# Kernel optimization log

Hardware: AMD Instinct MI355X
Metric: run time of the kernel (lower is better)

## Reference

```python
import jax, jax.numpy as jnp
import numpy as np

PATCH = 64
STRIDE = PATCH // 2
SEQ = 65536
NPATCH = (SEQ - PATCH) // STRIDE + 1  # 2047
B = 256
EPS = 1e-5


def setup_inputs() -> dict:
    key = jax.random.key(0)
    ks = jax.random.split(key, 10)
    s = lambda k, shp: jax.random.normal(k, shp, jnp.float32) * 0.05
    return dict(
        x=jax.random.normal(ks[0], (B, 1, SEQ), jnp.float32),
        conv1_w=s(ks[1], (NPATCH, NPATCH - 1)),
        conv1_b=s(ks[2], (NPATCH,)),
        w1=s(ks[3], (32, 3, 5)), b1=s(ks[4], (32,)),
        g1=jnp.ones((32,), jnp.float32), be1=jnp.zeros((32,), jnp.float32),
        w2=s(ks[5], (64, 32, 3)), b2=s(ks[6], (64,)),
        g2=jnp.ones((64,), jnp.float32), be2=jnp.zeros((64,), jnp.float32),
        w3=s(ks[7], (128, 64, 3)), b3=s(ks[8], (128,)),
        g3=jnp.ones((128,), jnp.float32), be3=jnp.zeros((128,), jnp.float32),
    )


def _conv1d(x, w, b, pad):
    # x: [B, Cin, L], w: [Cout, Cin, K]
    y = jax.lax.conv_general_dilated(x, w, (1,), [(pad, pad)],
                                     dimension_numbers=('NCH', 'OIH', 'NCH'))
    return y + b[None, :, None]


def _bn(x, g, be):
    # training-mode BatchNorm1d: biased var over (batch, length)
    m = jnp.mean(x, axis=(0, 2), keepdims=True)
    v = jnp.var(x, axis=(0, 2), keepdims=True)
    return (x - m) * jax.lax.rsqrt(v + EPS) * g[None, :, None] + be[None, :, None]


def _maxpool2(x):
    # MaxPool1d(kernel=2, stride=2), floor division of length
    L = x.shape[-1] // 2
    return x[..., : 2 * L].reshape(x.shape[0], x.shape[1], L, 2).max(-1)


def reference(x, conv1_w, conv1_b, w1, b1, g1, be1, w2, b2, g2, be2, w3, b3, g3, be3):
    starts = jnp.arange(NPATCH) * STRIDE
    idx = starts[:, None] + jnp.arange(PATCH)[None, :]         # [NW, W]
    xp = x[:, :, idx]                                          # [B,1,NW,W]
    mean = xp.mean(-1)                                         # [B,1,NW]
    std = jnp.std(xp, axis=-1, ddof=1)                         # torch.std is unbiased
    stats = jnp.concatenate([mean, std], axis=1)               # [B,2,NW]
    dx = jnp.diff(xp, axis=2)                                  # diff across window index: [B,1,NW-1,W]
    dmax = dx.max(-1)                                          # [B,1,NW-1]
    dmax = jnp.transpose(dmax, (0, 2, 1))                      # [B,NW-1,1]
    # conv1: 1x1 Conv1d over length-1 axis == matmul over channel dim
    d2 = jnp.einsum('oi,bil->bol', conv1_w, dmax) + conv1_b[None, :, None]  # [B,NW,1]
    d2 = jnp.transpose(d2, (0, 2, 1))                          # [B,1,NW]
    x3 = jnp.concatenate([stats, d2], axis=1)                  # [B,3,NW]
    h = _maxpool2(jax.nn.relu(_bn(_conv1d(x3, w1, b1, 2), g1, be1)))
    h = _maxpool2(jax.nn.relu(_bn(_conv1d(h, w2, b2, 1), g2, be2)))
    h = jax.nn.relu(_bn(_conv1d(h, w3, b3, 1), g3, be3))
    return h.mean(-1)                                          # AdaptiveAvgPool1d(1)+Flatten -> [B,128]
```

## Files before the change

kernel.cpp:

```cpp
#include <hip/hip_runtime.h>
#include <math.h>

#define NB 256
#define SEQ 65536
#define NP 2047
#define NPM 2046
#define NPP 2048
#define KPAD 2048
#define LEN1 2047
#define LEN2 1023
#define LEN3 511
#define C1 32
#define C2 64
#define C3 128
#define NPART 2048
#define NPART2 (NB*4)
#define SROW 40
#define SROW3 72

#define OFF_X3   0
#define SZ_X3    (NB*3*NPP)
#define OFF_DMAX (OFF_X3 + SZ_X3)
#define SZ_DMAX  (NB*NPM)
#define OFF_Y1   (OFF_DMAX + SZ_DMAX)
#define SZ_Y1    (NB*C1*LEN1)
#define OFF_Y2   (OFF_Y1 + SZ_Y1)
#define SZ_Y2    (NB*C2*LEN2)
#define OFF_S1   (OFF_Y2 + SZ_Y2)
#define OFF_S2   (OFF_S1 + 2*C1)
#define OFF_S3   (OFF_S2 + 2*C2)
#define OFF_W2C  (OFF_S3 + 2*C3)
#define OFF_W3B  (OFF_W2C + C1*C2*3)
#define OFF_PS   (OFF_W3B + C2*C3*3)
#define OFF_PQ   (OFF_PS + C3*NPART)
#define OFF_WB   OFF_Y2
#define OFF_H1R  OFF_Y2
#define OFF_PM   (OFF_Y1 + 4300000)
#define OFF_W2B  OFF_W2C

typedef __attribute__((ext_vector_type(8))) short short8;
typedef __attribute__((ext_vector_type(4))) short short4v;
typedef __attribute__((ext_vector_type(4))) float f32x4;

__device__ inline short f2bf(float f){
  union { float f; unsigned u; } x; x.f = f;
  unsigned r = x.u + 0x7FFF + ((x.u >> 16) & 1);
  return (short)(r >> 16);
}
__device__ inline float bf2f(short s){
  union { unsigned u; float f; } x; x.u = ((unsigned)(unsigned short)s) << 16; return x.f;
}

#define RED4L(v) v += __shfl_xor(v,1,64); v += __shfl_xor(v,2,64); \
                 v += __shfl_xor(v,4,64); v += __shfl_xor(v,8,64);

#define TILES(X) X(0,0) X(0,1) X(0,2) X(0,3) X(1,0) X(1,1) X(1,2) X(1,3) \
                 X(2,0) X(2,1) X(2,2) X(2,3) X(3,0) X(3,1) X(3,2) X(3,3)
#define DECLBIAS(P,ct) f32x4 bi##ct = *(const f32x4*)((P) + cbase + ct*16 + kq*4);
#define DECLACC(lt,ct) f32x4 acc##lt##ct = bi##ct;

__global__ __launch_bounds__(256) void k_pp(const float* __restrict__ x, const float* __restrict__ c1b,
                                            const float* __restrict__ W, const float* __restrict__ w2,
                                            const float* __restrict__ w3, float* __restrict__ ws){
  int bid = blockIdx.x;
  if (bid < 32*NB){
    float* x3    = ws + OFF_X3;
    short* dmaxB = (short*)(ws + OFF_DMAX);
    int b = bid >> 5;
    int chunk = bid & 31;
    const float* xr = x + (size_t)b*SEQ + chunk*2048;
    __shared__ float Ss[65], Qs[65], Dm[65];
    int w = threadIdx.x >> 6;
    int l = threadIdx.x & 63;
    #pragma unroll
    for (int i=0;i<2;i++){
      int seg = w*2 + i;
      int off = seg*256;
      float4 A = *(const float4*)(xr + off + l*4);
      float4 Bh = make_float4(0.f,0.f,0.f,0.f);
      if (l >= 56){
        int g = chunk*2048 + off + 256 + (l-56)*4;
        if (g + 3 < SEQ) Bh = *(const float4*)(xr + off + 256 + (l-56)*4);
      }
      int src = (l+8) & 63;
      float p0 = __shfl(A.x, src, 64), p1 = __shfl(A.y, src, 64),
            p2 = __shfl(A.z, src, 64), p3 = __shfl(A.w, src, 64);
      if (l >= 56){ p0=Bh.x; p1=Bh.y; p2=Bh.z; p3=Bh.w; }
      float s = (A.x+A.y)+(A.z+A.w);
      float q = fmaf(A.x,A.x, fmaf(A.y,A.y, fmaf(A.z,A.z, A.w*A.w)));
      float d = fmaxf(fmaxf(p0-A.x, p1-A.y), fmaxf(p2-A.z, p3-A.w));
      #pragma unroll
      for (int o=1;o<8;o<<=1){
        s += __shfl_xor(s,o,64);
        q += __shfl_xor(q,o,64);
        d  = fmaxf(d, __shfl_xor(d,o,64));
      }
      if ((l&7)==0){ int m = seg*8 + (l>>3); Ss[m]=s; Qs[m]=q; Dm[m]=d; }
    }
    if (w==0){
      float s=0.f,q=0.f,d=-1e30f;
      if (l < 8){
        int g = chunk*2048 + 2048 + l*4;
        if (g+3 < SEQ){
          float4 A = *(const float4*)(xr + 2048 + l*4);
          float4 P = make_float4(0.f,0.f,0.f,0.f);
          if (g+35 < SEQ) P = *(const float4*)(xr + 2048 + 32 + l*4);
          s = (A.x+A.y)+(A.z+A.w);
          q = fmaf(A.x,A.x, fmaf(A.y,A.y, fmaf(A.z,A.z, A.w*A.w)));
          d = fmaxf(fmaxf(P.x-A.x, P.y-A.y), fmaxf(P.z-A.z, P.w-A.w));
        }
      }
      #pragma unroll
      for (int o=1;o<8;o<<=1){
        s += __shfl_xor(s,o,64);
        q += __shfl_xor(q,o,64);
        d  = fmaxf(d, __shfl_xor(d,o,64));
      }
      if (l==0){ Ss[64]=s; Qs[64]=q; Dm[64]=d; }
    }
    __syncthreads();
    if (threadIdx.x < 64){
      int j = threadIdx.x;
      int p = chunk*64 + j;
      if (p < NP){
        float S = Ss[j]+Ss[j+1];
        float Q = Qs[j]+Qs[j+1];
        float mean = S*(1.0f/64.0f);
        float var  = (Q - S*mean)*(1.0f/63.0f);
        x3[(size_t)(b*3+0)*NPP + p] = mean;
        x3[(size_t)(b*3+1)*NPP + p] = sqrtf(fmaxf(var,0.0f));
        x3[(size_t)(b*3+2)*NPP + p] = c1b[p];
      }
      dmaxB[(size_t)b*KPAD + p] = (p < NPM) ? f2bf(fmaxf(Dm[j], Dm[j+1])) : (short)0;
    }
  } else {
    int pb = bid - 32*NB;
    if (pb < 8*NP){
      short* Wb = (short*)(ws + OFF_WB);
      int o = pb >> 3;
      int k = (pb & 7)*256 + threadIdx.x;
      Wb[(size_t)o*KPAD + k] = (k < NPM) ? f2bf(W[(size_t)o*NPM + k]) : (short)0;
    } else {
      short* w2b = (short*)(ws + OFF_W2B);
      short* w3b = (short*)(ws + OFF_W3B);
      int t = (pb - 8*NP)*256 + threadIdx.x;
      if (t < 3*C2*C1){
        int tap = t / (C2*C1);
        int r = t - tap*(C2*C1);
        int c = r >> 5, i = r & 31;
        w2b[t] = f2bf(w2[(c*C1 + i)*3 + tap]);
      }
      if (t < 3*C3*C2){
        int tap = t / (C3*C2);
        int r = t - tap*(C3*C2);
        int c = r / C2, i = r - c*C2;
        w3b[(tap*C3 + c)*C2 + i] = f2bf(w3[(c*C2+i)*3 + tap]);
      }
    }
  }
}

__global__ __launch_bounds__(256) void k_gemm(float* __restrict__ ws){
  const short* Ab = (const short*)(ws + OFF_DMAX);
  const short* Bb = (const short*)(ws + OFF_WB);
  float* x3 = ws + OFF_X3;
  int wid  = __builtin_amdgcn_readfirstlane(threadIdx.x >> 6);
  int lane = threadIdx.x & 63;
  int ln = lane & 15, kq = lane >> 4;
  int n0  = blockIdx.x*32;
  int ks  = blockIdx.y*512;
  f32x4 acc[4][2];
  #pragma unroll
  for (int bt=0;bt<4;bt++){ acc[bt][0] = (f32x4){0.f,0.f,0.f,0.f}; acc[bt][1] = (f32x4){0.f,0.f,0.f,0.f}; }
  int o0 = n0 + ln, o1 = n0 + 16 + ln;
  const short* ap  = Ab + (size_t)(wid*16 + ln)*KPAD + ks + kq*8;
  const short* bp0 = Bb + (size_t)min(o0, NP-1)*KPAD + ks + kq*8;
  const short* bp1 = Bb + (size_t)min(o1, NP-1)*KPAD + ks + kq*8;
  #pragma unroll 2
  for (int s=0; s<16; s++){
    short8 b0 = *(const short8*)(bp0 + s*32);
    short8 b1 = *(const short8*)(bp1 + s*32);
    #pragma unroll
    for (int bt=0;bt<4;bt++){
      short8 av = *(const short8*)(ap + (size_t)bt*64*KPAD + s*32);
      acc[bt][0] = __builtin_amdgcn_mfma_f32_16x16x32_bf16(av, b0, acc[bt][0], 0, 0, 0);
      acc[bt][1] = __builtin_amdgcn_mfma_f32_16x16x32_bf16(av, b1, acc[bt][1], 0, 0, 0);
    }
  }
  #pragma unroll
  for (int bt=0;bt<4;bt++){
    #pragma unroll
    for (int r=0;r<4;r++){
      int b = bt*64 + wid*16 + kq*4 + r;
      float* xp = x3 + ((size_t)(b*3) + 2)*NPP;
      if (o0 < NP) atomicAdd(xp + o0, acc[bt][0][r]);
      if (o1 < NP) atomicAdd(xp + o1, acc[bt][1][r]);
    }
  }
}

__global__ __launch_bounds__(256) void k_conv1f(const float* __restrict__ w1, const float* __restrict__ b1, float* __restrict__ ws){
  const float* x3 = ws + OFF_X3;
  short* h1rB = (short*)(ws + OFF_H1R);
  float* ps = ws + OFF_PS;
  float* pq = ws + OFF_PQ;
  int b = blockIdx.y;
  int blk = blockIdx.x;
  int w = threadIdx.x >> 6;
  int lane = threadIdx.x & 63;
  int h = lane >> 5, c = lane & 31;
  int p0 = blk*256 + w*64 + h*32;
  float wv[3][5];
  #pragma unroll
  for (int i=0;i<3;i++){
    #pragma unroll
    for (int j=0;j<5;j++) wv[i][j] = w1[(c*3+i)*5+j];
  }
  float bc = b1[c];
  const float* xb = x3 + (size_t)b*3*NPP;
  float s = 0.f, q = 0.f;
  #pragma unroll
  for (int k0=0;k0<32;k0+=8){
    int base = p0 + k0 - 4;
    float xw[3][16];
    #pragma unroll
    for (int i=0;i<3;i++){
      const float* xr = xb + (size_t)i*NPP;
      if (base >= 0 && base + 16 <= LEN1){
        #pragma unroll
        for (int t=0;t<4;t++) *(f32x4*)&xw[i][4*t] = *(const f32x4*)(xr + base + 4*t);
      } else {
        #pragma unroll
        for (int t=0;t<16;t++){ int g = base + t; xw[i][t] = (g >= 0 && g < LEN1) ? xr[g] : 0.f; }
      }
    }
    float acc[8];
    #pragma unroll
    for (int k=0;k<8;k++){
      float a = bc;
      #pragma unroll
      for (int i=0;i<3;i++){
        #pragma unroll
        for (int j=0;j<5;j++) a = fmaf(wv[i][j], xw[i][k+j+2], a);
      }
      acc[k] = a;
      if (p0 + k0 + k < LEN1){ s += a; q = fmaf(a, a, q); }
    }
    #pragma unroll
    for (int t=0;t<4;t++){
      int m = ((p0 + k0) >> 1) + t;
      if (m < LEN2) h1rB[((size_t)b*LEN2 + m)*C1 + c] = f2bf(fmaxf(acc[2*t], acc[2*t+1]));
    }
  }
  s += __shfl_xor(s, 32, 64);
  q += __shfl_xor(q, 32, 64);
  __shared__ float es[4][C1], eq[4][C1];
  if (h == 0){ es[w][c] = s; eq[w][c] = q; }
  __syncthreads();
  if (threadIdx.x < C1){
    int cc = threadIdx.x;
    float S = es[0][cc]+es[1][cc]+es[2][cc]+es[3][cc];
    float Q = eq[0][cc]+eq[1][cc]+eq[2][cc]+eq[3][cc];
    ps[(size_t)cc*NPART + b*8 + blk] = S;
    pq[(size_t)cc*NPART + b*8 + blk] = Q;
  }
}

__global__ __launch_bounds__(256) void k_fin(const float* __restrict__ ps, const float* __restrict__ pq,
                                             const float* __restrict__ g, const float* __restrict__ be,
                                             float* __restrict__ stats, int C, int npart, double invN,
                                             float* __restrict__ outz){
  if (outz) outz[(size_t)threadIdx.x * C3 + blockIdx.x] = 0.f;
  int c = blockIdx.x;
  double s=0.0, q=0.0;
  for (int j=threadIdx.x; j<npart; j+=256){ s += (double)ps[c*npart+j]; q += (double)pq[c*npart+j]; }
  #pragma unroll
  for (int off=32; off; off>>=1){ s += __shfl_xor(s,off,64); q += __shfl_xor(q,off,64); }
  __shared__ double rs[4], rq[4];
  int wid = threadIdx.x>>6, lane=threadIdx.x&63;
  if (lane==0){ rs[wid]=s; rq[wid]=q; }
  __syncthreads();
  if (threadIdx.x==0){
    double S = rs[0]+rs[1]+rs[2]+rs[3];
    double Q = rq[0]+rq[1]+rq[2]+rq[3];
    double mean = S*invN;
    double var  = Q*invN - mean*mean;
    double a = (double)g[c] / sqrt(var + 1e-5);
    stats[c]   = (float)a;
    stats[C+c] = (float)((double)be[c] - mean*a);
  }
}

__global__ __launch_bounds__(256) void k_conv2m(const float* __restrict__ b2, float* __restrict__ ws){
  const short* h1rB = (const short*)(ws + OFF_H1R);
  const float* st1 = ws + OFF_S1;
  const short* w2b = (const short*)(ws + OFF_W2B);
  short* pmB = (short*)(ws + OFF_PM);
  float* ps = ws + OFF_PS;
  float* pq = ws + OFF_PQ;
  int b   = blockIdx.y;
  int blk = blockIdx.x;
  int l0  = blk*256;
  __shared__ __align__(16) short sh[258*SROW];
  for (int u = threadIdx.x; u < 258*4; u += 256){
    int row = u >> 2, g = u & 3;
    int pos = l0 - 1 + row;
    short8 r8 = (short8)0;
    if (pos >= 0 && pos < LEN2){
      short8 xv = *(const short8*)(h1rB + ((size_t)b*LEN2 + pos)*C1 + g*8);
      f32x4 alo = *(const f32x4*)(st1 + g*8),      ahi = *(const f32x4*)(st1 + g*8 + 4);
      f32x4 blo = *(const f32x4*)(st1 + C1 + g*8), bhi = *(const f32x4*)(st1 + C1 + g*8 + 4);
      #pragma unroll
      for (int j=0;j<4;j++){
        r8[j]   = f2bf(fmaxf(fmaf(alo[j], bf2f(xv[j]),   blo[j]), 0.f));
        r8[j+4] = f2bf(fmaxf(fmaf(ahi[j], bf2f(xv[j+4]), bhi[j]), 0.f));
      }
    }
    *(short8*)(sh + row*SROW + g*8) = r8;
  }
  __syncthreads();
  int w   = __builtin_amdgcn_readfirstlane(threadIdx.x >> 6);
  int lane = threadIdx.x & 63;
  int ln = lane & 15, kq = lane >> 4;
  int lw = l0 + w*64;
  int cbase = 0;
  DECLBIAS(b2,0) DECLBIAS(b2,1) DECLBIAS(b2,2) DECLBIAS(b2,3)
  TILES(DECLACC)
  const short* wA = w2b + (size_t)ln*C1 + kq*8;
#define LDW(T,ct) short8 aw##T##ct = *(const short8*)(wA + (size_t)(T*C2 + ct*16)*C1);
  LDW(0,0) LDW(0,1) LDW(0,2) LDW(0,3)
  LDW(1,0) LDW(1,1) LDW(1,2) LDW(1,3)
  LDW(2,0) LDW(2,1) LDW(2,2) LDW(2,3)
#undef LDW
#define MMT0(lt,ct) acc##lt##ct = __builtin_amdgcn_mfma_f32_16x16x32_bf16(aw0##ct, bv##lt, acc##lt##ct, 0, 0, 0);
#define MMT1(lt,ct) acc##lt##ct = __builtin_amdgcn_mfma_f32_16x16x32_bf16(aw1##ct, bv##lt, acc##lt##ct, 0, 0, 0);
#define MMT2(lt,ct) acc##lt##ct = __builtin_amdgcn_mfma_f32_16x16x32_bf16(aw2##ct, bv##lt, acc##lt##ct, 0, 0, 0);
#define LDB2(lt,T) short8 bv##lt = *(const short8*)(sh + (size_t)(w*64 + lt*16 + T + ln)*SROW + kq*8);
#define CSTEP(T) { LDB2(0,T) LDB2(1,T) LDB2(2,T) LDB2(3,T) TILES(MMT##T) }
  CSTEP(0) CSTEP(1) CSTEP(2)
#undef CSTEP
#undef LDB2
#define PST(lt,ct) { \
    float p0_ = fmaxf(acc##lt##ct[0], __shfl_xor(acc##lt##ct[0],1,64)); \
    float p1_ = fmaxf(acc##lt##ct[1], __shfl_xor(acc##lt##ct[1],1,64)); \
    float p2_ = fmaxf(acc##lt##ct[2], __shfl_xor(acc##lt##ct[2],1,64)); \
    float p3_ = fmaxf(acc##lt##ct[3], __shfl_xor(acc##lt##ct[3],1,64)); \
    int l_ = lw + lt*16 + ln; \
    if (!(ln & 1) && (l_ >> 1) < LEN3){ \
      short4v pv_ = { f2bf(p0_), f2bf(p1_), f2bf(p2_), f2bf(p3_) }; \
      *(short4v*)(pmB + ((size_t)b*LEN3 + (l_>>1))*C2 + ct*16 + kq*4) = pv_; } }
  TILES(PST)
#undef PST
  __shared__ float es[4][C2], eq[4][C2];
  #pragma unroll
  for (int ct=0;ct<4;ct++){
    float s0=0.f,s1=0.f,s2=0.f,s3=0.f,q0=0.f,q1=0.f,q2=0.f,q3=0.f;
#define ACCST(lt,CT) if (CT == ct){ int l_ = lw + lt*16 + ln; if (l_ < LEN2){ \
      s0 += acc##lt##CT[0]; q0 = fmaf(acc##lt##CT[0], acc##lt##CT[0], q0); \
      s1 += acc##lt##CT[1]; q1 = fmaf(acc##lt##CT[1], acc##lt##CT[1], q1); \
      s2 += acc##lt##CT[2]; q2 = fmaf(acc##lt##CT[2], acc##lt##CT[2], q2); \
      s3 += acc##lt##CT[3]; q3 = fmaf(acc##lt##CT[3], acc##lt##CT[3], q3); } }
    TILES(ACCST)
#undef ACCST
    RED4L(s0) RED4L(s1) RED4L(s2) RED4L(s3)
    RED4L(q0) RED4L(q1) RED4L(q2) RED4L(q3)
    if (ln == 0){
      int c0 = ct*16 + kq*4;
      es[w][c0+0]=s0; es[w][c0+1]=s1; es[w][c0+2]=s2; es[w][c0+3]=s3;
      eq[w][c0+0]=q0; eq[w][c0+1]=q1; eq[w][c0+2]=q2; eq[w][c0+3]=q3;
    }
  }
  __syncthreads();
  if (threadIdx.x < C2){
    int c = threadIdx.x;
    float S = es[0][c]+es[1][c]+es[2][c]+es[3][c];
    float Q = eq[0][c]+eq[1][c]+eq[2][c]+eq[3][c];
    ps[(size_t)c*NPART2 + b*4 + blk] = S;
    pq[(size_t)c*NPART2 + b*4 + blk] = Q;
  }
}

#define STAGE3(SH, BB, L0BLK) \
  for (int u = threadIdx.x; u < 130*8; u += 256){ \
    int row_ = u >> 3, g_ = u & 7; \
    int pos_ = (L0BLK) - 1 + row_; \
    short8 r8_ = (short8)0; \
    if (pos_ >= 0 && pos_ < LEN3){ \
      short8 xm_ = *(const short8*)(pmB + ((size_t)(BB)*LEN3 + pos_)*C2 + g_*8); \
      f32x4 alo_ = *(const f32x4*)(st2 + g_*8),      ahi_ = *(const f32x4*)(st2 + g_*8 + 4); \
      f32x4 blo_ = *(const f32x4*)(st2 + C2 + g_*8), bhi_ = *(const f32x4*)(st2 + C2 + g_*8 + 4); \
      _Pragma("unroll") \
      for (int j=0;j<4;j++){ \
        r8_[j]   = f2bf(fmaxf(fmaf(alo_[j], bf2f(xm_[j]),   blo_[j]), 0.f)); \
        r8_[j+4] = f2bf(fmaxf(fmaf(ahi_[j], bf2f(xm_[j+4]), bhi_[j]), 0.f)); \
      } \
    } \
    *(short8*)(SH + (size_t)row_*SROW3 + g_*8) = r8_; \
  }

__global__ __launch_bounds__(256) void k_conv3s(const float* __restrict__ b3, float* __restrict__ ws){
  const short* pmB = (const short*)(ws + OFF_PM);
  const float* st2 = ws + OFF_S2;
  const short* w3b = (const short*)(ws + OFF_W3B);
  float* ps = ws + OFF_PS;
  float* pq = ws + OFF_PQ;
  int b   = blockIdx.y;
  int blk = blockIdx.x;
  int l0blk = blk*128;
  __shared__ __align__(16) short sh[130*SROW3];
  STAGE3(sh, b, l0blk)
  __syncthreads();
  int wid = __builtin_amdgcn_readfirstlane(threadIdx.x >> 6);
  int lane = threadIdx.x & 63;
  int ln = lane & 15, kq = lane >> 4;
  int lh = wid & 1, ch = wid >> 1;
  int l0 = l0blk + lh*64;
  int cbase = ch*64;
  DECLBIAS(b3,0) DECLBIAS(b3,1) DECLBIAS(b3,2) DECLBIAS(b3,3)
  TILES(DECLACC)
  const short* hL = sh + (size_t)(lh*64 + ln)*SROW3 + kq*8;
  const short* wA = w3b + (size_t)(cbase + ln)*C2 + kq*8;
  #pragma unroll
  for (int t=0;t<3;t++){
    #pragma unroll
    for (int s=0;s<2;s++){
#define LDB(lt) short8 bv##lt = *(const short8*)(hL + (size_t)(lt*16 + t)*SROW3 + s*32);
      LDB(0) LDB(1) LDB(2) LDB(3)
#define LDA(ct) short8 av##ct = *(const short8*)(wA + (size_t)(t*C3 + ct*16)*C2 + s*32);
      LDA(0) LDA(1) LDA(2) LDA(3)
#define MM(lt,ct) acc##lt##ct = __builtin_amdgcn_mfma_f32_16x16x32_bf16(av##ct, bv##lt, acc##lt##ct, 0, 0, 0);
      TILES(MM)
#undef LDB
#undef LDA
    }
  }
  int pidx = b*8 + blk*2 + lh;
  #pragma unroll
  for (int ct=0;ct<4;ct++){
    float s0=0.f,s1=0.f,s2=0.f,s3=0.f,q0=0.f,q1=0.f,q2=0.f,q3=0.f;
#define ACCST(lt,CT) if (CT == ct){ int l_ = l0 + lt*16 + ln; if (l_ < LEN3){ \
      s0 += acc##lt##CT[0]; q0 = fmaf(acc##lt##CT[0], acc##lt##CT[0], q0); \
      s1 += acc##lt##CT[1]; q1 = fmaf(acc##lt##CT[1], acc##lt##CT[1], q1); \
      s2 += acc##lt##CT[2]; q2 = fmaf(acc##lt##CT[2], acc##lt##CT[2], q2); \
      s3 += acc##lt##CT[3]; q3 = fmaf(acc##lt##CT[3], acc##lt##CT[3], q3); } }
    TILES(ACCST)
#undef ACCST
    RED4L(s0) RED4L(s1) RED4L(s2) RED4L(s3)
    RED4L(q0) RED4L(q1) RED4L(q2) RED4L(q3)
    if (ln == 0){
      int c0 = cbase + ct*16 + kq*4;
      ps[(size_t)(c0+0)*NPART + pidx] = s0;  pq[(size_t)(c0+0)*NPART + pidx] = q0;
      ps[(size_t)(c0+1)*NPART + pidx] = s1;  pq[(size_t)(c0+1)*NPART + pidx] = q1;
      ps[(size_t)(c0+2)*NPART + pidx] = s2;  pq[(size_t)(c0+2)*NPART + pidx] = q2;
      ps[(size_t)(c0+3)*NPART + pidx] = s3;  pq[(size_t)(c0+3)*NPART + pidx] = q3;
    }
  }
}

__global__ __launch_bounds__(256) void k_out3(float* __restrict__ out, const float* __restrict__ b3,
                                              const float* __restrict__ ws){
  const short* pmB = (const short*)(ws + OFF_PM);
  const float* st2 = ws + OFF_S2;
  const short* w3b = (const short*)(ws + OFF_W3B);
  const float* st  = ws + OFF_S3;
  int b   = blockIdx.y;
  int blk = blockIdx.x;
  int l0blk = blk*128;
  __shared__ __align__(16) short sh[130*SROW3];
  STAGE3(sh, b, l0blk)
  __syncthreads();
  int wid = __builtin_amdgcn_readfirstlane(threadIdx.x >> 6);
  int lane = threadIdx.x & 63;
  int ln = lane & 15, kq = lane >> 4;
  int lh = wid & 1, ch = wid >> 1;
  int l0 = l0blk + lh*64;
  int cbase = ch*64;
  DECLBIAS(b3,0) DECLBIAS(b3,1) DECLBIAS(b3,2) DECLBIAS(b3,3)
  TILES(DECLACC)
  const short* hL = sh + (size_t)(lh*64 + ln)*SROW3 + kq*8;
  const short* wA = w3b + (size_t)(cbase + ln)*C2 + kq*8;
  #pragma unroll
  for (int t=0;t<3;t++){
    #pragma unroll
    for (int s=0;s<2;s++){
#define LDB(lt) short8 bv##lt = *(const short8*)(hL + (size_t)(lt*16 + t)*SROW3 + s*32);
      LDB(0) LDB(1) LDB(2) LDB(3)
#define LDA(ct) short8 av##ct = *(const short8*)(wA + (size_t)(t*C3 + ct*16)*C2 + s*32);
      LDA(0) LDA(1) LDA(2) LDA(3)
      TILES(MM)
#undef LDB
#undef LDA
    }
  }
  const float inv = 1.0f/511.0f;
  #pragma unroll
  for (int ct=0;ct<4;ct++){
    int c0 = cbase + ct*16 + kq*4;
    float a0 = st[c0+0], a1 = st[c0+1], a2 = st[c0+2], a3 = st[c0+3];
    float h0 = st[C3+c0+0], h1_ = st[C3+c0+1], h2_ = st[C3+c0+2], h3 = st[C3+c0+3];
    float s0=0.f,s1=0.f,s2=0.f,s3=0.f;
#define OSUM(lt,CT) if (CT == ct){ int l_ = l0 + lt*16 + ln; if (l_ < LEN3){ \
      s0 += fmaxf(fmaf(a0, acc##lt##CT[0], h0 ), 0.f); \
      s1 += fmaxf(fmaf(a1, acc##lt##CT[1], h1_), 0.f); \
      s2 += fmaxf(fmaf(a2, acc##lt##CT[2], h2_), 0.f); \
      s3 += fmaxf(fmaf(a3, acc##lt##CT[3], h3 ), 0.f); } }
    TILES(OSUM)
#undef OSUM
    RED4L(s0) RED4L(s1) RED4L(s2) RED4L(s3)
    if (ln == 0){
      atomicAdd(out + (size_t)b*C3 + c0+0, s0*inv);
      atomicAdd(out + (size_t)b*C3 + c0+1, s1*inv);
      atomicAdd(out + (size_t)b*C3 + c0+2, s2*inv);
      atomicAdd(out + (size_t)b*C3 + c0+3, s3*inv);
    }
  }
}

extern "C" void kernel_launch(void* const* d_in, const int* in_sizes, int n_in,
                              void* d_out, int out_size, void* d_ws, size_t ws_size,
                              hipStream_t stream) {
  const float* x   = (const float*)d_in[0];
  const float* c1w = (const float*)d_in[1];
  const float* c1b = (const float*)d_in[2];
  const float* w1  = (const float*)d_in[3];
  const float* b1  = (const float*)d_in[4];
  const float* g1  = (const float*)d_in[5];
  const float* be1 = (const float*)d_in[6];
  const float* w2  = (const float*)d_in[7];
  const float* b2  = (const float*)d_in[8];
  const float* g2  = (const float*)d_in[9];
  const float* be2 = (const float*)d_in[10];
  const float* w3  = (const float*)d_in[11];
  const float* b3  = (const float*)d_in[12];
  const float* g3  = (const float*)d_in[13];
  const float* be3 = (const float*)d_in[14];
  float* ws  = (float*)d_ws;
  float* out = (float*)d_out;

  hipLaunchKernelGGL(k_pp,     dim3(32*NB + 8*NP + 96), dim3(256), 0, stream, x, c1b, c1w, w2, w3, ws);
  hipLaunchKernelGGL(k_gemm,   dim3(64,4), dim3(256), 0, stream, ws);
  hipLaunchKernelGGL(k_conv1f, dim3(8,NB), dim3(256), 0, stream, w1, b1, ws);
  hipLaunchKernelGGL(k_fin,    dim3(C1), dim3(256), 0, stream, ws+OFF_PS, ws+OFF_PQ, g1, be1, ws+OFF_S1, C1, NPART, 1.0/((double)NB*LEN1), (float*)nullptr);
  hipLaunchKernelGGL(k_conv2m, dim3(4,NB), dim3(256), 0, stream, b2, ws);
  hipLaunchKernelGGL(k_fin,    dim3(C2), dim3(256), 0, stream, ws+OFF_PS, ws+OFF_PQ, g2, be2, ws+OFF_S2, C2, NPART2, 1.0/((double)NB*LEN2), (float*)nullptr);
  hipLaunchKernelGGL(k_conv3s, dim3(4,NB), dim3(256), 0, stream, b3, ws);
  hipLaunchKernelGGL(k_fin,    dim3(C3), dim3(256), 0, stream, ws+OFF_PS, ws+OFF_PQ, g3, be3, ws+OFF_S3, C3, NPART, 1.0/((double)NB*LEN3), out);
  hipLaunchKernelGGL(k_out3,   dim3(4,NB), dim3(256), 0, stream, out, b3, ws);
}
```

Before: 258.7 us.

## Stage patch windows in LDS per thread and split GEMM K further

The patch-statistics stage is restructured. Each block now covers 256 patches: it stages an 8288-float input window in padded shared memory, and each thread computes one patch's sum, sum of squares and diff-max serially from that window using a 32-entry ring buffer. This replaces the earlier warp-shuffle reduction over 2048-sample chunks. Separately, the dmax GEMM splits K into 8 slices of 256 instead of 4 of 512, doubling the grid and the atomic adds. The aim is fewer preprocessing blocks and less shuffle overhead, plus more GEMM parallelism; the cost is a serial 96-step loop per thread with strided LDS reads, and more atomic traffic.

```diff
diff --git a/kernel.cpp b/kernel.cpp
--- a/kernel.cpp
+++ b/kernel.cpp
@@ -17,6 +17,8 @@
 #define NPART2 (NB*4)
 #define SROW 40
 #define SROW3 72
+#define PWIN 8288
+#define PLDS (PWIN + PWIN/32 + 2)
 
 #define OFF_X3   0
 #define SZ_X3    (NB*3*NPP)
@@ -63,78 +65,55 @@
                                             const float* __restrict__ W, const float* __restrict__ w2,
                                             const float* __restrict__ w3, float* __restrict__ ws){
   int bid = blockIdx.x;
-  if (bid < 32*NB){
+  if (bid < 8*NB){
     float* x3    = ws + OFF_X3;
     short* dmaxB = (short*)(ws + OFF_DMAX);
-    int b = bid >> 5;
-    int chunk = bid & 31;
-    const float* xr = x + (size_t)b*SEQ + chunk*2048;
-    __shared__ float Ss[65], Qs[65], Dm[65];
-    int w = threadIdx.x >> 6;
-    int l = threadIdx.x & 63;
-    #pragma unroll
-    for (int i=0;i<2;i++){
-      int seg = w*2 + i;
-      int off = seg*256;
-      float4 A = *(const float4*)(xr + off + l*4);
-      float4 Bh = make_float4(0.f,0.f,0.f,0.f);
-      if (l >= 56){
-        int g = chunk*2048 + off + 256 + (l-56)*4;
-        if (g + 3 < SEQ) Bh = *(const float4*)(xr + off + 256 + (l-56)*4);
+    int b   = bid >> 3;
+    int blk = bid & 7;
+    int P0  = blk*256;
+    __shared__ float xs[PLDS];
+    const float* xb = x + (size_t)b*SEQ + (size_t)P0*32;
+    int lim = SEQ - P0*32;
+    for (int u = threadIdx.x; u < PWIN/4; u += 256){
+      int i0 = u*4;
+      float4 v;
+      if (i0 + 4 <= lim){
+        v = *(const float4*)(xb + i0);
+      } else {
+        float t0 = (i0+0 < lim) ? xb[i0+0] : 0.f;
+        float t1 = (i0+1 < lim) ? xb[i0+1] : 0.f;
+        float t2 = (i0+2 < lim) ? xb[i0+2] : 0.f;
+        float t3 = (i0+3 < lim) ? xb[i0+3] : 0.f;
+        v = make_float4(t0,t1,t2,t3);
       }
-      int src = (l+8) & 63;
-      float p0 = __shfl(A.x, src, 64), p1 = __shfl(A.y, src, 64),
-            p2 = __shfl(A.z, src, 64), p3 = __shfl(A.w, src, 64);
-      if (l >= 56){ p0=Bh.x; p1=Bh.y; p2=Bh.z; p3=Bh.w; }
-      float s = (A.x+A.y)+(A.z+A.w);
-      float q = fmaf(A.x,A.x, fmaf(A.y,A.y, fmaf(A.z,A.z, A.w*A.w)));
-      float d = fmaxf(fmaxf(p0-A.x, p1-A.y), fmaxf(p2-A.z, p3-A.w));
-      #pragma unroll
-      for (int o=1;o<8;o<<=1){
-        s += __shfl_xor(s,o,64);
-        q += __shfl_xor(q,o,64);
-        d  = fmaxf(d, __shfl_xor(d,o,64));
-      }
-      if ((l&7)==0){ int m = seg*8 + (l>>3); Ss[m]=s; Qs[m]=q; Dm[m]=d; }
-    }
-    if (w==0){
-      float s=0.f,q=0.f,d=-1e30f;
-      if (l < 8){
-        int g = chunk*2048 + 2048 + l*4;
-        if (g+3 < SEQ){
-          float4 A = *(const float4*)(xr + 2048 + l*4);
-          float4 P = make_float4(0.f,0.f,0.f,0.f);
-          if (g+35 < SEQ) P = *(const float4*)(xr + 2048 + 32 + l*4);
-          s = (A.x+A.y)+(A.z+A.w);
-          q = fmaf(A.x,A.x, fmaf(A.y,A.y, fmaf(A.z,A.z, A.w*A.w)));
-          d = fmaxf(fmaxf(P.x-A.x, P.y-A.y), fmaxf(P.z-A.z, P.w-A.w));
-        }
-      }
-      #pragma unroll
-      for (int o=1;o<8;o<<=1){
-        s += __shfl_xor(s,o,64);
-        q += __shfl_xor(q,o,64);
-        d  = fmaxf(d, __shfl_xor(d,o,64));
-      }
-      if (l==0){ Ss[64]=s; Qs[64]=q; Dm[64]=d; }
+      int i;
+      i = i0+0; xs[i + (i>>5)] = v.x;
+      i = i0+1; xs[i + (i>>5)] = v.y;
+      i = i0+2; xs[i + (i>>5)] = v.z;
+      i = i0+3; xs[i + (i>>5)] = v.w;
     }
     __syncthreads();
-    if (threadIdx.x < 64){
-      int j = threadIdx.x;
-      int p = chunk*64 + j;
-      if (p < NP){
-        float S = Ss[j]+Ss[j+1];
-        float Q = Qs[j]+Qs[j+1];
-        float mean = S*(1.0f/64.0f);
-        float var  = (Q - S*mean)*(1.0f/63.0f);
-        x3[(size_t)(b*3+0)*NPP + p] = mean;
-        x3[(size_t)(b*3+1)*NPP + p] = sqrtf(fmaxf(var,0.0f));
-        x3[(size_t)(b*3+2)*NPP + p] = c1b[p];
-      }
-      dmaxB[(size_t)b*KPAD + p] = (p < NPM) ? f2bf(fmaxf(Dm[j], Dm[j+1])) : (short)0;
-    }
+    int t = threadIdx.x;
+    int p = P0 + t;
+    float ring[32];
+    float s = 0.f, q = 0.f, d = -1e30f;
+    #pragma unroll
+    for (int j=0;j<96;j++){
+      float v = xs[33*t + j + (j>>5)];
+      if (j < 64){ s += v; q = fmaf(v, v, q); }
+      if (j >= 32){ d = fmaxf(d, v - ring[j & 31]); }
+      ring[j & 31] = v;
+    }
+    if (p < NP){
+      float mean = s*(1.0f/64.0f);
+      float var  = (q - s*mean)*(1.0f/63.0f);
+      x3[(size_t)(b*3+0)*NPP + p] = mean;
+      x3[(size_t)(b*3+1)*NPP + p] = sqrtf(fmaxf(var,0.0f));
+      x3[(size_t)(b*3+2)*NPP + p] = c1b[p];
+    }
+    dmaxB[(size_t)b*KPAD + p] = (p < NPM) ? f2bf(d) : (short)0;
   } else {
-    int pb = bid - 32*NB;
+    int pb = bid - 8*NB;
     if (pb < 8*NP){
       short* Wb = (short*)(ws + OFF_WB);
       int o = pb >> 3;
@@ -168,7 +147,7 @@
   int lane = threadIdx.x & 63;
   int ln = lane & 15, kq = lane >> 4;
   int n0  = blockIdx.x*32;
-  int ks  = blockIdx.y*512;
+  int ks  = blockIdx.y*256;
   f32x4 acc[4][2];
   #pragma unroll
   for (int bt=0;bt<4;bt++){ acc[bt][0] = (f32x4){0.f,0.f,0.f,0.f}; acc[bt][1] = (f32x4){0.f,0.f,0.f,0.f}; }
@@ -177,7 +156,7 @@
   const short* bp0 = Bb + (size_t)min(o0, NP-1)*KPAD + ks + kq*8;
   const short* bp1 = Bb + (size_t)min(o1, NP-1)*KPAD + ks + kq*8;
   #pragma unroll 2
-  for (int s=0; s<16; s++){
+  for (int s=0; s<8; s++){
     short8 b0 = *(const short8*)(bp0 + s*32);
     short8 b1 = *(const short8*)(bp1 + s*32);
     #pragma unroll
@@ -537,8 +516,8 @@
   float* ws  = (float*)d_ws;
   float* out = (float*)d_out;
 
-  hipLaunchKernelGGL(k_pp,     dim3(32*NB + 8*NP + 96), dim3(256), 0, stream, x, c1b, c1w, w2, w3, ws);
-  hipLaunchKernelGGL(k_gemm,   dim3(64,4), dim3(256), 0, stream, ws);
+  hipLaunchKernelGGL(k_pp,     dim3(8*NB + 8*NP + 96), dim3(256), 0, stream, x, c1b, c1w, w2, w3, ws);
+  hipLaunchKernelGGL(k_gemm,   dim3(64,8), dim3(256), 0, stream, ws);
   hipLaunchKernelGGL(k_conv1f, dim3(8,NB), dim3(256), 0, stream, w1, b1, ws);
   hipLaunchKernelGGL(k_fin,    dim3(C1), dim3(256), 0, stream, ws+OFF_PS, ws+OFF_PQ, g1, be1, ws+OFF_S1, C1, NPART, 1.0/((double)NB*LEN1), (float*)nullptr);
   hipLaunchKernelGGL(k_conv2m, dim3(4,NB), dim3(256), 0, stream, b2, ws);
```

Measured after the change: 270.6 us. 4.6% more time.
